# Performance work log

Measured on AMD Instinct MI355X. Metric: run time of the kernel, lower is better.

The kernel has to match this reference:

```python
import jax, jax.numpy as jnp
import numpy as np

B, S, D_MODEL, H = 2, 2048, 768, 12
HD = D_MODEL // H  # head_dim = 64
EPS = 1e-5


def setup_inputs() -> dict:
    key = jax.random.key(0)
    ks = jax.random.split(key, 5)
    sc = 0.02
    return {
        "x": jax.random.normal(ks[0], (B, S, D_MODEL), dtype=jnp.float32),
        "Wproj_w": jax.random.normal(ks[1], (7 * D_MODEL, D_MODEL), dtype=jnp.float32) * sc,
        "Wproj_b": jax.random.normal(ks[2], (7 * D_MODEL,), dtype=jnp.float32) * sc,
        "gn_w": jnp.ones((D_MODEL,), dtype=jnp.float32),
        "gn_b": jnp.zeros((D_MODEL,), dtype=jnp.float32),
        "out_w": jax.random.normal(ks[3], (D_MODEL, D_MODEL), dtype=jnp.float32) * sc,
        "out_b": jax.random.normal(ks[4], (D_MODEL,), dtype=jnp.float32) * sc,
    }


def _time_swiglu(qkv):
    # qkv: [B, S, 7, H, D]
    q1, k1, q2, k2, q3, k3, v = [qkv[:, :, i] for i in range(7)]
    a1 = jnp.einsum('bthd,bshd->bhts', q1, k1)  # [B,H,S,S], raw scores, no softmax
    a2 = jnp.einsum('bthd,bshd->bhts', q2, k2)
    a3 = jnp.einsum('bthd,bshd->bhts', q3, k3)
    t1 = jax.nn.silu(jnp.einsum('bhts,bshd->bthd', a1, v))
    t2 = jnp.einsum('bhts,bshd->bthd', a2, v)
    return jnp.einsum('bhts,bshd->bthd', a3, t1 * t2)  # [B,S,H,D]


def _group_norm(ctx, gn_w, gn_b):
    # ctx: [B, S, D_MODEL]; torch applies GroupNorm(H, D_MODEL) over (B, C=D_MODEL, L=S)
    g = ctx.reshape(B, S, H, HD)
    mean = jnp.mean(g, axis=(1, 3), keepdims=True)          # per (batch, group) over (S, HD)
    var = jnp.var(g, axis=(1, 3), keepdims=True)
    g = (g - mean) * jax.lax.rsqrt(var + EPS)
    g = g.reshape(B, S, D_MODEL)
    return g * gn_w + gn_b


def reference(x, Wproj_w, Wproj_b, gn_w, gn_b, out_w, out_b):
    qkv = x @ Wproj_w.T + Wproj_b                  # [B,S,7*D_MODEL]
    qkv = qkv.reshape(B, S, 7, H, HD)
    ctx = _time_swiglu(qkv).reshape(B, S, D_MODEL)  # [B,S,D_MODEL]
    ctx = _group_norm(ctx, gn_w, gn_b)
    return ctx @ out_w.T + out_b
```

## Files before the change

### kernel.cpp

```cpp
#include <hip/hip_runtime.h>
#include <hip/hip_bf16.h>
#include <stdint.h>

typedef short short8 __attribute__((ext_vector_type(8)));
typedef float f32x4 __attribute__((ext_vector_type(4)));
typedef unsigned short u16x4 __attribute__((ext_vector_type(4)));

#define MFMA16 __builtin_amdgcn_mfma_f32_16x16x32_bf16

typedef unsigned int __attribute__((address_space(1))) as1_u32;
typedef unsigned int __attribute__((address_space(3))) as3_u32;
#define GLOAD16(gsrc, ldst) \
  __builtin_amdgcn_global_load_lds((const as1_u32*)(gsrc), (as3_u32*)(ldst), 16, 0, 0)

__device__ __forceinline__ unsigned short f2bf(float f) {
  __hip_bfloat16 h = __float2bfloat16(f);
  return *(unsigned short*)&h;
}

__global__ __launch_bounds__(256) void cvt_bf16_4(const float* __restrict__ in,
                                                  unsigned short* __restrict__ out,
                                                  int n) {
  int i = (blockIdx.x * 256 + threadIdx.x) * 4;
  if (i >= n) return;
  f32x4 v = *(const f32x4*)(in + i);
  u16x4 o;
  o.x = f2bf(v.x); o.y = f2bf(v.y); o.z = f2bf(v.z); o.w = f2bf(v.w);
  *(u16x4*)(out + i) = o;
}

__global__ __launch_bounds__(256) void transp64(const unsigned short* __restrict__ src,
                                                int stride, int off,
                                                unsigned short* __restrict__ dst) {
  __shared__ __align__(16) unsigned short t[64 * 64];
  const int tid = threadIdx.x;
  const int tt = blockIdx.x, bh = blockIdx.y;
  const int b = bh / 12, h = bh % 12;
  const unsigned short* sbase = src + (size_t)(b * 2048 + tt * 64) * stride + h * 64 + off;
  for (int it = 0; it < 2; ++it) {
    int slot = it * 256 + tid, s = slot >> 3, j = slot & 7;
    short8 v = *(const short8*)(sbase + (size_t)s * stride + j * 8);
    int phys = (s + 8 * j) & 63;
    for (int e = 0; e < 8; ++e)
      t[(j * 8 + e) * 64 + phys] = ((unsigned short*)&v)[e];
  }
  __syncthreads();
  unsigned short* dbase = dst + (size_t)bh * 64 * 2048 + tt * 64;
  for (int it = 0; it < 2; ++it) {
    int slot = it * 256 + tid, d = slot >> 3, c = slot & 7;
    int pc = (c + (d >> 3)) & 7;
    short8 v = *(const short8*)(t + d * 64 + pc * 8);
    *(short8*)(dbase + (size_t)d * 2048 + c * 8) = v;
  }
}

template <bool OUT_BF16>
__global__ __launch_bounds__(256) void gemm_nt(const unsigned short* __restrict__ A,
                                               const unsigned short* __restrict__ Bm,
                                               const float* __restrict__ bias,
                                               void* __restrict__ Cout,
                                               int M, int N, int K) {
  __shared__ __align__(16) char smem[32768];
  char* As = smem;
  char* Bs = smem + 16384;
  const int tid = threadIdx.x;
  const int w = tid >> 6, l = tid & 63;
  const int wm = w >> 1, wn = w & 1;
  const int Row0 = blockIdx.y * 128, Col0 = blockIdx.x * 128;

  f32x4 z; z.x = 0.f; z.y = 0.f; z.z = 0.f; z.w = 0.f;
  f32x4 acc[4][4];
  for (int m = 0; m < 4; ++m)
    for (int n = 0; n < 4; ++n) acc[m][n] = z;

  for (int k0 = 0; k0 < K; k0 += 64) {
    for (int it = 0; it < 4; ++it) {
      int slot = it * 256 + tid;
      int row = slot >> 3, j = slot & 7;
      int gc = j ^ (row & 7);
      GLOAD16(A + (size_t)(Row0 + row) * K + k0 + gc * 8, As + slot * 16);
      GLOAD16(Bm + (size_t)(Col0 + row) * K + k0 + gc * 8, Bs + slot * 16);
    }
    __syncthreads();
    for (int kc = 0; kc < 2; ++kc) {
      int c = (l >> 4) + 4 * kc;
      short8 af[4], bf[4];
      for (int m = 0; m < 4; ++m) {
        int t = wm * 64 + m * 16 + (l & 15);
        af[m] = *(const short8*)(As + t * 128 + ((c ^ (t & 7)) * 16));
      }
      for (int n = 0; n < 4; ++n) {
        int t = wn * 64 + n * 16 + (l & 15);
        bf[n] = *(const short8*)(Bs + t * 128 + ((c ^ (t & 7)) * 16));
      }
      for (int m = 0; m < 4; ++m)
        for (int n = 0; n < 4; ++n)
          acc[m][n] = MFMA16(af[m], bf[n], acc[m][n], 0, 0, 0);
    }
    __syncthreads();
  }
  for (int n = 0; n < 4; ++n) {
    int col = Col0 + wn * 64 + n * 16 + (l & 15);
    float bv = bias[col];
    for (int m = 0; m < 4; ++m) {
      int rbase = Row0 + wm * 64 + m * 16 + (l >> 4) * 4;
      for (int r = 0; r < 4; ++r) {
        float v = acc[m][n][r] + bv;
        size_t idx = (size_t)(rbase + r) * N + col;
        if (OUT_BF16) ((unsigned short*)Cout)[idx] = f2bf(v);
        else          ((float*)Cout)[idx] = v;
      }
    }
  }
}

__global__ __launch_bounds__(256) void pass1(const unsigned short* __restrict__ qkv,
                                             const unsigned short* __restrict__ vt,
                                             unsigned short* __restrict__ u) {
  __shared__ __align__(16) char smem[40960];
  char* K1s = smem;
  char* K2s = smem + 8192;
  char* Vts = smem + 16384;
  char* A1s = smem + 24576;
  char* A2s = smem + 32768;
  const int tid = threadIdx.x, w = tid >> 6, l = tid & 63;
  const int tt = blockIdx.x;
  const int bh = blockIdx.y;
  const int b = bh / 12, h = bh % 12;

  const int tg = tt * 64 + w * 16 + (l & 15);
  const size_t qbase = (size_t)(b * 2048 + tg) * 5376 + h * 64;
  short8 q1f[2], q2f[2];
  for (int kc = 0; kc < 2; ++kc) {
    int d = kc * 32 + (l >> 4) * 8;
    q1f[kc] = *(const short8*)(qkv + qbase + 0 * 768 + d);
    q2f[kc] = *(const short8*)(qkv + qbase + 2 * 768 + d);
  }

  f32x4 z; z.x = 0.f; z.y = 0.f; z.z = 0.f; z.w = 0.f;
  f32x4 t1a[4], t2a[4];
  for (int n = 0; n < 4; ++n) { t1a[n] = z; t2a[n] = z; }

  for (int s0 = 0; s0 < 2048; s0 += 64) {
    for (int it = 0; it < 2; ++it) {
      int slot = it * 256 + tid;
      int row = slot >> 3, j = slot & 7;
      int gc = j ^ (row & 7);
      const unsigned short* k1src = qkv + (size_t)(b * 2048 + s0 + row) * 5376 + h * 64 + 768 + gc * 8;
      GLOAD16(k1src, K1s + slot * 16);
      GLOAD16(k1src + 2 * 768, K2s + slot * 16);
      GLOAD16(vt + (size_t)(bh * 64 + row) * 2048 + s0 + gc * 8, Vts + slot * 16);
    }
    __syncthreads();

    f32x4 a1[4], a2[4];
    for (int n = 0; n < 4; ++n) { a1[n] = z; a2[n] = z; }
    for (int kc = 0; kc < 2; ++kc) {
      int c = (l >> 4) + 4 * kc;
      for (int n = 0; n < 4; ++n) {
        int srw = n * 16 + (l & 15);
        short8 k1f = *(const short8*)(K1s + srw * 128 + ((c ^ (srw & 7)) * 16));
        short8 k2f = *(const short8*)(K2s + srw * 128 + ((c ^ (srw & 7)) * 16));
        a1[n] = MFMA16(q1f[kc], k1f, a1[n], 0, 0, 0);
        a2[n] = MFMA16(q2f[kc], k2f, a2[n], 0, 0, 0);
      }
    }

    char* myA1 = A1s + w * 2048;
    char* myA2 = A2s + w * 2048;
    for (int n = 0; n < 4; ++n)
      for (int r = 0; r < 4; ++r) {
        int trow = (l >> 4) * 4 + r;
        int scol = n * 16 + (l & 15);
        int byte = trow * 128 + (((scol >> 3) ^ (trow & 7)) * 16) + (scol & 7) * 2;
        *(unsigned short*)(myA1 + byte) = f2bf(a1[n][r]);
        *(unsigned short*)(myA2 + byte) = f2bf(a2[n][r]);
      }
    __syncthreads();

    for (int kc = 0; kc < 2; ++kc) {
      int trow = l & 15;
      int c = (l >> 4) + 4 * kc;
      short8 p1 = *(const short8*)(myA1 + trow * 128 + ((c ^ (trow & 7)) * 16));
      short8 p2 = *(const short8*)(myA2 + trow * 128 + ((c ^ (trow & 7)) * 16));
      for (int n = 0; n < 4; ++n) {
        int drow = n * 16 + (l & 15);
        short8 vf = *(const short8*)(Vts + drow * 128 + ((c ^ (drow & 7)) * 16));
        t1a[n] = MFMA16(p1, vf, t1a[n], 0, 0, 0);
        t2a[n] = MFMA16(p2, vf, t2a[n], 0, 0, 0);
      }
    }
    __syncthreads();
  }

  for (int n = 0; n < 4; ++n)
    for (int r = 0; r < 4; ++r) {
      int t = tt * 64 + w * 16 + (l >> 4) * 4 + r;
      int d = n * 16 + (l & 15);
      float x1 = t1a[n][r], x2 = t2a[n][r];
      float uu = (x1 / (1.f + expf(-x1))) * x2;
      u[(size_t)(b * 2048 + t) * 768 + h * 64 + d] = f2bf(uu);
    }
}

__global__ __launch_bounds__(256) void pass2(const unsigned short* __restrict__ qkv,
                                             const unsigned short* __restrict__ ut,
                                             float* __restrict__ ctx,
                                             float* __restrict__ partials) {
  __shared__ __align__(16) char smem[24576];
  char* K3s = smem;
  char* Uts = smem + 8192;
  char* A3s = smem + 16384;
  const int tid = threadIdx.x, w = tid >> 6, l = tid & 63;
  const int tt = blockIdx.x;
  const int bh = blockIdx.y;
  const int b = bh / 12, h = bh % 12;

  const int tg = tt * 64 + w * 16 + (l & 15);
  const size_t qbase = (size_t)(b * 2048 + tg) * 5376 + h * 64;
  short8 q3f[2];
  for (int kc = 0; kc < 2; ++kc)
    q3f[kc] = *(const short8*)(qkv + qbase + 4 * 768 + kc * 32 + (l >> 4) * 8);

  f32x4 z; z.x = 0.f; z.y = 0.f; z.z = 0.f; z.w = 0.f;
  f32x4 ca[4];
  for (int n = 0; n < 4; ++n) ca[n] = z;

  for (int s0 = 0; s0 < 2048; s0 += 64) {
    for (int it = 0; it < 2; ++it) {
      int slot = it * 256 + tid;
      int row = slot >> 3, j = slot & 7;
      int gc = j ^ (row & 7);
      GLOAD16(qkv + (size_t)(b * 2048 + s0 + row) * 5376 + h * 64 + 5 * 768 + gc * 8,
              K3s + slot * 16);
      GLOAD16(ut + (size_t)(bh * 64 + row) * 2048 + s0 + gc * 8, Uts + slot * 16);
    }
    __syncthreads();

    f32x4 a3[4];
    for (int n = 0; n < 4; ++n) a3[n] = z;
    for (int kc = 0; kc < 2; ++kc) {
      int c = (l >> 4) + 4 * kc;
      for (int n = 0; n < 4; ++n) {
        int srw = n * 16 + (l & 15);
        short8 kf = *(const short8*)(K3s + srw * 128 + ((c ^ (srw & 7)) * 16));
        a3[n] = MFMA16(q3f[kc], kf, a3[n], 0, 0, 0);
      }
    }
    char* myA = A3s + w * 2048;
    for (int n = 0; n < 4; ++n)
      for (int r = 0; r < 4; ++r) {
        int trow = (l >> 4) * 4 + r;
        int scol = n * 16 + (l & 15);
        int byte = trow * 128 + (((scol >> 3) ^ (trow & 7)) * 16) + (scol & 7) * 2;
        *(unsigned short*)(myA + byte) = f2bf(a3[n][r]);
      }
    __syncthreads();

    for (int kc = 0; kc < 2; ++kc) {
      int trow = l & 15;
      int c = (l >> 4) + 4 * kc;
      short8 p3 = *(const short8*)(myA + trow * 128 + ((c ^ (trow & 7)) * 16));
      for (int n = 0; n < 4; ++n) {
        int drow = n * 16 + (l & 15);
        short8 uf = *(const short8*)(Uts + drow * 128 + ((c ^ (drow & 7)) * 16));
        ca[n] = MFMA16(p3, uf, ca[n], 0, 0, 0);
      }
    }
    __syncthreads();
  }

  float psum = 0.f, psum2 = 0.f;
  for (int n = 0; n < 4; ++n)
    for (int r = 0; r < 4; ++r) {
      int t = tt * 64 + w * 16 + (l >> 4) * 4 + r;
      int d = n * 16 + (l & 15);
      float v = ca[n][r];
      ctx[(size_t)(b * 2048 + t) * 768 + h * 64 + d] = v;
      psum += v; psum2 += v * v;
    }

  float* red = (float*)smem;
  red[tid] = psum; red[256 + tid] = psum2;
  __syncthreads();
  for (int st = 128; st > 0; st >>= 1) {
    if (tid < st) {
      red[tid] += red[tid + st];
      red[256 + tid] += red[256 + tid + st];
    }
    __syncthreads();
  }
  if (tid == 0) {
    partials[(bh * 32 + tt) * 2] = red[0];
    partials[(bh * 32 + tt) * 2 + 1] = red[256];
  }
}

__global__ __launch_bounds__(64) void gn_finalize(const float* __restrict__ partials,
                                                  float* __restrict__ stats) {
  const int g = blockIdx.x;
  const int l = threadIdx.x;
  double s = 0.0, s2 = 0.0;
  if (l < 32) {
    s = (double)partials[(g * 32 + l) * 2];
    s2 = (double)partials[(g * 32 + l) * 2 + 1];
  }
  for (int off = 32; off > 0; off >>= 1) {
    s += __shfl_down(s, off, 64);
    s2 += __shfl_down(s2, off, 64);
  }
  if (l == 0) {
    const double N = 2048.0 * 64.0;
    double mean = s / N;
    double var = s2 / N - mean * mean;
    stats[g * 2] = (float)mean;
    stats[g * 2 + 1] = (float)(1.0 / sqrt(var + 1e-5));
  }
}

__global__ __launch_bounds__(256) void gn_apply(const float* __restrict__ ctx,
                                                const float* __restrict__ stats,
                                                const float* __restrict__ gw,
                                                const float* __restrict__ gb,
                                                unsigned short* __restrict__ outc) {
  int i = blockIdx.x * 256 + threadIdx.x;
  if (i >= 4096 * 768) return;
  int c = i % 768;
  int b = i / (2048 * 768);
  int g = b * 12 + (c >> 6);
  float v = (ctx[i] - stats[2 * g]) * stats[2 * g + 1];
  outc[i] = f2bf(v * gw[c] + gb[c]);
}

extern "C" void kernel_launch(void* const* d_in, const int* in_sizes, int n_in,
                              void* d_out, int out_size, void* d_ws, size_t ws_size,
                              hipStream_t stream) {
  const float* x   = (const float*)d_in[0];
  const float* Wpw = (const float*)d_in[1];
  const float* Wpb = (const float*)d_in[2];
  const float* gnw = (const float*)d_in[3];
  const float* gnb = (const float*)d_in[4];
  const float* ow  = (const float*)d_in[5];
  const float* ob  = (const float*)d_in[6];
  float* out = (float*)d_out;

  char* ws = (char*)d_ws;
  size_t off = 0;
  auto carve = [&](size_t bytes) {
    char* p = ws + off;
    off = (off + bytes + 255) & ~(size_t)255;
    return p;
  };
  unsigned short* xb   = (unsigned short*)carve((size_t)4096 * 768 * 2);
  unsigned short* wb   = (unsigned short*)carve((size_t)5376 * 768 * 2);
  unsigned short* owb  = (unsigned short*)carve((size_t)768 * 768 * 2);
  unsigned short* qkvb = (unsigned short*)carve((size_t)4096 * 5376 * 2);
  unsigned short* ub   = (unsigned short*)carve((size_t)4096 * 768 * 2);
  unsigned short* vtb  = (unsigned short*)carve((size_t)24 * 64 * 2048 * 2);
  unsigned short* utb  = (unsigned short*)carve((size_t)24 * 64 * 2048 * 2);
  float* ctx           = (float*)carve((size_t)4096 * 768 * 4);
  float* partials      = (float*)carve(24 * 32 * 2 * 4);
  float* stats         = (float*)carve(48 * 4);

  cvt_bf16_4<<<3072, 256, 0, stream>>>(x, xb, 4096 * 768);
  cvt_bf16_4<<<4032, 256, 0, stream>>>(Wpw, wb, 5376 * 768);
  cvt_bf16_4<<<576, 256, 0, stream>>>(ow, owb, 768 * 768);

  gemm_nt<true><<<dim3(42, 32), 256, 0, stream>>>(xb, wb, Wpb, qkvb, 4096, 5376, 768);
  transp64<<<dim3(32, 24), 256, 0, stream>>>(qkvb, 5376, 6 * 768, vtb);
  pass1<<<dim3(32, 24), 256, 0, stream>>>(qkvb, vtb, ub);
  transp64<<<dim3(32, 24), 256, 0, stream>>>(ub, 768, 0, utb);
  pass2<<<dim3(32, 24), 256, 0, stream>>>(qkvb, utb, ctx, partials);
  gn_finalize<<<24, 64, 0, stream>>>(partials, stats);
  gn_apply<<<12288, 256, 0, stream>>>(ctx, stats, gnw, gnb, xb);
  gemm_nt<false><<<dim3(6, 32), 256, 0, stream>>>(xb, owb, ob, out, 4096, 768, 768);
}
```

Measured before the change: 238.1 us.

## Switch attention passes to 32x32 MFMA with 128-row query tiles per block

Both attention passes move from 16x16x32 to 32x32x16 bf16 MFMA. Each wave now owns 32 query rows, so a block covers 128 rows and the grid halves from 32 to 16 tiles per head. Each staged K/V/U tile is therefore reused across twice as many queries, and global traffic per output is lower. The score tile is computed transposed (K as the A operand) so it can be written to LDS as packed 64-bit stores. The mid-loop block barrier is replaced by a per-wave lgkmcnt wait, since each wave only reads its own score region. The trade-off is fewer blocks (384), more LDS per block and more accumulator registers, which may reduce occupancy.

```diff
diff --git a/kernel.cpp b/kernel.cpp
--- a/kernel.cpp
+++ b/kernel.cpp
@@ -4,9 +4,11 @@
 
 typedef short short8 __attribute__((ext_vector_type(8)));
 typedef float f32x4 __attribute__((ext_vector_type(4)));
+typedef float f32x16 __attribute__((ext_vector_type(16)));
 typedef unsigned short u16x4 __attribute__((ext_vector_type(4)));
 
 #define MFMA16 __builtin_amdgcn_mfma_f32_16x16x32_bf16
+#define MFMA32 __builtin_amdgcn_mfma_f32_32x32x16_bf16
 
 typedef unsigned int __attribute__((address_space(1))) as1_u32;
 typedef unsigned int __attribute__((address_space(3))) as3_u32;
@@ -16,6 +18,9 @@
 __device__ __forceinline__ unsigned short f2bf(float f) {
   __hip_bfloat16 h = __float2bfloat16(f);
   return *(unsigned short*)&h;
+}
+__device__ __forceinline__ unsigned pk2(float lo, float hi) {
+  return ((unsigned)f2bf(hi) << 16) | (unsigned)f2bf(lo);
 }
 
 __global__ __launch_bounds__(256) void cvt_bf16_4(const float* __restrict__ in,
@@ -117,87 +122,103 @@
 __global__ __launch_bounds__(256) void pass1(const unsigned short* __restrict__ qkv,
                                              const unsigned short* __restrict__ vt,
                                              unsigned short* __restrict__ u) {
-  __shared__ __align__(16) char smem[40960];
+  __shared__ __align__(16) char smem[57344];
   char* K1s = smem;
   char* K2s = smem + 8192;
   char* Vts = smem + 16384;
   char* A1s = smem + 24576;
-  char* A2s = smem + 32768;
+  char* A2s = smem + 40960;
   const int tid = threadIdx.x, w = tid >> 6, l = tid & 63;
-  const int tt = blockIdx.x;
-  const int bh = blockIdx.y;
+  const int g5 = l >> 5, l31 = l & 31;
+  const int tt = blockIdx.x, bh = blockIdx.y;
   const int b = bh / 12, h = bh % 12;
 
-  const int tg = tt * 64 + w * 16 + (l & 15);
-  const size_t qbase = (size_t)(b * 2048 + tg) * 5376 + h * 64;
-  short8 q1f[2], q2f[2];
-  for (int kc = 0; kc < 2; ++kc) {
-    int d = kc * 32 + (l >> 4) * 8;
-    q1f[kc] = *(const short8*)(qkv + qbase + 0 * 768 + d);
-    q2f[kc] = *(const short8*)(qkv + qbase + 2 * 768 + d);
-  }
-
-  f32x4 z; z.x = 0.f; z.y = 0.f; z.z = 0.f; z.w = 0.f;
-  f32x4 t1a[4], t2a[4];
-  for (int n = 0; n < 4; ++n) { t1a[n] = z; t2a[n] = z; }
+  const int tg = tt * 128 + w * 32 + l31;
+  const unsigned short* qrow = qkv + (size_t)(b * 2048 + tg) * 5376 + h * 64;
+  short8 q1f[4], q2f[4];
+#pragma unroll
+  for (int kc = 0; kc < 4; ++kc) {
+    int d = kc * 16 + g5 * 8;
+    q1f[kc] = *(const short8*)(qrow + 0 * 768 + d);
+    q2f[kc] = *(const short8*)(qrow + 2 * 768 + d);
+  }
+
+  f32x16 z16;
+#pragma unroll
+  for (int i = 0; i < 16; ++i) z16[i] = 0.f;
+  f32x16 t1a[2], t2a[2];
+  t1a[0] = z16; t1a[1] = z16; t2a[0] = z16; t2a[1] = z16;
+
+  char* myA1 = A1s + w * 4096;
+  char* myA2 = A2s + w * 4096;
 
   for (int s0 = 0; s0 < 2048; s0 += 64) {
+#pragma unroll
     for (int it = 0; it < 2; ++it) {
       int slot = it * 256 + tid;
       int row = slot >> 3, j = slot & 7;
       int gc = j ^ (row & 7);
-      const unsigned short* k1src = qkv + (size_t)(b * 2048 + s0 + row) * 5376 + h * 64 + 768 + gc * 8;
-      GLOAD16(k1src, K1s + slot * 16);
-      GLOAD16(k1src + 2 * 768, K2s + slot * 16);
+      const unsigned short* ksrc =
+          qkv + (size_t)(b * 2048 + s0 + row) * 5376 + h * 64 + 768 + gc * 8;
+      GLOAD16(ksrc, K1s + slot * 16);
+      GLOAD16(ksrc + 2 * 768, K2s + slot * 16);
       GLOAD16(vt + (size_t)(bh * 64 + row) * 2048 + s0 + gc * 8, Vts + slot * 16);
     }
     __syncthreads();
 
-    f32x4 a1[4], a2[4];
-    for (int n = 0; n < 4; ++n) { a1[n] = z; a2[n] = z; }
-    for (int kc = 0; kc < 2; ++kc) {
-      int c = (l >> 4) + 4 * kc;
-      for (int n = 0; n < 4; ++n) {
-        int srw = n * 16 + (l & 15);
-        short8 k1f = *(const short8*)(K1s + srw * 128 + ((c ^ (srw & 7)) * 16));
-        short8 k2f = *(const short8*)(K2s + srw * 128 + ((c ^ (srw & 7)) * 16));
-        a1[n] = MFMA16(q1f[kc], k1f, a1[n], 0, 0, 0);
-        a2[n] = MFMA16(q2f[kc], k2f, a2[n], 0, 0, 0);
-      }
-    }
-
-    char* myA1 = A1s + w * 2048;
-    char* myA2 = A2s + w * 2048;
-    for (int n = 0; n < 4; ++n)
-      for (int r = 0; r < 4; ++r) {
-        int trow = (l >> 4) * 4 + r;
-        int scol = n * 16 + (l & 15);
-        int byte = trow * 128 + (((scol >> 3) ^ (trow & 7)) * 16) + (scol & 7) * 2;
-        *(unsigned short*)(myA1 + byte) = f2bf(a1[n][r]);
-        *(unsigned short*)(myA2 + byte) = f2bf(a2[n][r]);
-      }
-    __syncthreads();
-
-    for (int kc = 0; kc < 2; ++kc) {
-      int trow = l & 15;
-      int c = (l >> 4) + 4 * kc;
-      short8 p1 = *(const short8*)(myA1 + trow * 128 + ((c ^ (trow & 7)) * 16));
-      short8 p2 = *(const short8*)(myA2 + trow * 128 + ((c ^ (trow & 7)) * 16));
-      for (int n = 0; n < 4; ++n) {
-        int drow = n * 16 + (l & 15);
-        short8 vf = *(const short8*)(Vts + drow * 128 + ((c ^ (drow & 7)) * 16));
-        t1a[n] = MFMA16(p1, vf, t1a[n], 0, 0, 0);
-        t2a[n] = MFMA16(p2, vf, t2a[n], 0, 0, 0);
-      }
-    }
-    __syncthreads();
-  }
-
-  for (int n = 0; n < 4; ++n)
-    for (int r = 0; r < 4; ++r) {
-      int t = tt * 64 + w * 16 + (l >> 4) * 4 + r;
-      int d = n * 16 + (l & 15);
-      float x1 = t1a[n][r], x2 = t2a[n][r];
+    f32x16 a1t[2], a2t[2];
+    a1t[0] = z16; a1t[1] = z16; a2t[0] = z16; a2t[1] = z16;
+#pragma unroll
+    for (int kc = 0; kc < 4; ++kc) {
+#pragma unroll
+      for (int n = 0; n < 2; ++n) {
+        int srow = n * 32 + l31;
+        int off = srow * 128 + (((kc * 2 + g5) ^ (srow & 7)) * 16);
+        a1t[n] = MFMA32(*(const short8*)(K1s + off), q1f[kc], a1t[n], 0, 0, 0);
+        a2t[n] = MFMA32(*(const short8*)(K2s + off), q2f[kc], a2t[n], 0, 0, 0);
+      }
+    }
+
+#pragma unroll
+    for (int n = 0; n < 2; ++n)
+#pragma unroll
+      for (int rq = 0; rq < 4; ++rq) {
+        int sbase = n * 32 + rq * 8 + g5 * 4;
+        int byte = l31 * 128 + (((sbase >> 3) ^ (l31 & 7)) * 16) + (sbase & 7) * 2;
+        uint2 w1, w2;
+        w1.x = pk2(a1t[n][rq * 4], a1t[n][rq * 4 + 1]);
+        w1.y = pk2(a1t[n][rq * 4 + 2], a1t[n][rq * 4 + 3]);
+        w2.x = pk2(a2t[n][rq * 4], a2t[n][rq * 4 + 1]);
+        w2.y = pk2(a2t[n][rq * 4 + 2], a2t[n][rq * 4 + 3]);
+        *(uint2*)(myA1 + byte) = w1;
+        *(uint2*)(myA2 + byte) = w2;
+      }
+    asm volatile("s_waitcnt lgkmcnt(0)" ::: "memory");
+
+#pragma unroll
+    for (int kc2 = 0; kc2 < 4; ++kc2) {
+      int chunk = kc2 * 2 + g5;
+      int aoff = l31 * 128 + ((chunk ^ (l31 & 7)) * 16);
+      short8 pa1 = *(const short8*)(myA1 + aoff);
+      short8 pa2 = *(const short8*)(myA2 + aoff);
+#pragma unroll
+      for (int dn = 0; dn < 2; ++dn) {
+        int drow = dn * 32 + l31;
+        short8 vf = *(const short8*)(Vts + drow * 128 + ((chunk ^ (drow & 7)) * 16));
+        t1a[dn] = MFMA32(pa1, vf, t1a[dn], 0, 0, 0);
+        t2a[dn] = MFMA32(pa2, vf, t2a[dn], 0, 0, 0);
+      }
+    }
+    __syncthreads();
+  }
+
+#pragma unroll
+  for (int dn = 0; dn < 2; ++dn)
+#pragma unroll
+    for (int r = 0; r < 16; ++r) {
+      int t = tt * 128 + w * 32 + (r & 3) + 8 * (r >> 2) + 4 * g5;
+      int d = dn * 32 + l31;
+      float x1 = t1a[dn][r], x2 = t2a[dn][r];
       float uu = (x1 / (1.f + expf(-x1))) * x2;
       u[(size_t)(b * 2048 + t) * 768 + h * 64 + d] = f2bf(uu);
     }
@@ -207,26 +228,31 @@
                                              const unsigned short* __restrict__ ut,
                                              float* __restrict__ ctx,
                                              float* __restrict__ partials) {
-  __shared__ __align__(16) char smem[24576];
+  __shared__ __align__(16) char smem[32768];
   char* K3s = smem;
   char* Uts = smem + 8192;
   char* A3s = smem + 16384;
   const int tid = threadIdx.x, w = tid >> 6, l = tid & 63;
-  const int tt = blockIdx.x;
-  const int bh = blockIdx.y;
+  const int g5 = l >> 5, l31 = l & 31;
+  const int tt = blockIdx.x, bh = blockIdx.y;
   const int b = bh / 12, h = bh % 12;
 
-  const int tg = tt * 64 + w * 16 + (l & 15);
-  const size_t qbase = (size_t)(b * 2048 + tg) * 5376 + h * 64;
-  short8 q3f[2];
-  for (int kc = 0; kc < 2; ++kc)
-    q3f[kc] = *(const short8*)(qkv + qbase + 4 * 768 + kc * 32 + (l >> 4) * 8);
-
-  f32x4 z; z.x = 0.f; z.y = 0.f; z.z = 0.f; z.w = 0.f;
-  f32x4 ca[4];
-  for (int n = 0; n < 4; ++n) ca[n] = z;
+  const int tg = tt * 128 + w * 32 + l31;
+  const unsigned short* qrow = qkv + (size_t)(b * 2048 + tg) * 5376 + h * 64;
+  short8 q3f[4];
+#pragma unroll
+  for (int kc = 0; kc < 4; ++kc)
+    q3f[kc] = *(const short8*)(qrow + 4 * 768 + kc * 16 + g5 * 8);
+
+  f32x16 z16;
+#pragma unroll
+  for (int i = 0; i < 16; ++i) z16[i] = 0.f;
+  f32x16 ca[2];
+  ca[0] = z16; ca[1] = z16;
+  char* myA = A3s + w * 4096;
 
   for (int s0 = 0; s0 < 2048; s0 += 64) {
+#pragma unroll
     for (int it = 0; it < 2; ++it) {
       int slot = it * 256 + tid;
       int row = slot >> 3, j = slot & 7;
@@ -237,45 +263,52 @@
     }
     __syncthreads();
 
-    f32x4 a3[4];
-    for (int n = 0; n < 4; ++n) a3[n] = z;
-    for (int kc = 0; kc < 2; ++kc) {
-      int c = (l >> 4) + 4 * kc;
-      for (int n = 0; n < 4; ++n) {
-        int srw = n * 16 + (l & 15);
-        short8 kf = *(const short8*)(K3s + srw * 128 + ((c ^ (srw & 7)) * 16));
-        a3[n] = MFMA16(q3f[kc], kf, a3[n], 0, 0, 0);
-      }
-    }
-    char* myA = A3s + w * 2048;
-    for (int n = 0; n < 4; ++n)
-      for (int r = 0; r < 4; ++r) {
-        int trow = (l >> 4) * 4 + r;
-        int scol = n * 16 + (l & 15);
-        int byte = trow * 128 + (((scol >> 3) ^ (trow & 7)) * 16) + (scol & 7) * 2;
-        *(unsigned short*)(myA + byte) = f2bf(a3[n][r]);
-      }
-    __syncthreads();
-
-    for (int kc = 0; kc < 2; ++kc) {
-      int trow = l & 15;
-      int c = (l >> 4) + 4 * kc;
-      short8 p3 = *(const short8*)(myA + trow * 128 + ((c ^ (trow & 7)) * 16));
-      for (int n = 0; n < 4; ++n) {
-        int drow = n * 16 + (l & 15);
-        short8 uf = *(const short8*)(Uts + drow * 128 + ((c ^ (drow & 7)) * 16));
-        ca[n] = MFMA16(p3, uf, ca[n], 0, 0, 0);
+    f32x16 a3t[2];
+    a3t[0] = z16; a3t[1] = z16;
+#pragma unroll
+    for (int kc = 0; kc < 4; ++kc) {
+#pragma unroll
+      for (int n = 0; n < 2; ++n) {
+        int srow = n * 32 + l31;
+        int off = srow * 128 + (((kc * 2 + g5) ^ (srow & 7)) * 16);
+        a3t[n] = MFMA32(*(const short8*)(K3s + off), q3f[kc], a3t[n], 0, 0, 0);
+      }
+    }
+#pragma unroll
+    for (int n = 0; n < 2; ++n)
+#pragma unroll
+      for (int rq = 0; rq < 4; ++rq) {
+        int sbase = n * 32 + rq * 8 + g5 * 4;
+        int byte = l31 * 128 + (((sbase >> 3) ^ (l31 & 7)) * 16) + (sbase & 7) * 2;
+        uint2 w1;
+        w1.x = pk2(a3t[n][rq * 4], a3t[n][rq * 4 + 1]);
+        w1.y = pk2(a3t[n][rq * 4 + 2], a3t[n][rq * 4 + 3]);
+        *(uint2*)(myA + byte) = w1;
+      }
+    asm volatile("s_waitcnt lgkmcnt(0)" ::: "memory");
+
+#pragma unroll
+    for (int kc2 = 0; kc2 < 4; ++kc2) {
+      int chunk = kc2 * 2 + g5;
+      short8 pa = *(const short8*)(myA + l31 * 128 + ((chunk ^ (l31 & 7)) * 16));
+#pragma unroll
+      for (int dn = 0; dn < 2; ++dn) {
+        int drow = dn * 32 + l31;
+        short8 uf = *(const short8*)(Uts + drow * 128 + ((chunk ^ (drow & 7)) * 16));
+        ca[dn] = MFMA32(pa, uf, ca[dn], 0, 0, 0);
       }
     }
     __syncthreads();
   }
 
   float psum = 0.f, psum2 = 0.f;
-  for (int n = 0; n < 4; ++n)
-    for (int r = 0; r < 4; ++r) {
-      int t = tt * 64 + w * 16 + (l >> 4) * 4 + r;
-      int d = n * 16 + (l & 15);
-      float v = ca[n][r];
+#pragma unroll
+  for (int dn = 0; dn < 2; ++dn)
+#pragma unroll
+    for (int r = 0; r < 16; ++r) {
+      int t = tt * 128 + w * 32 + (r & 3) + 8 * (r >> 2) + 4 * g5;
+      int d = dn * 32 + l31;
+      float v = ca[dn][r];
       ctx[(size_t)(b * 2048 + t) * 768 + h * 64 + d] = v;
       psum += v; psum2 += v * v;
     }
@@ -291,8 +324,8 @@
     __syncthreads();
   }
   if (tid == 0) {
-    partials[(bh * 32 + tt) * 2] = red[0];
-    partials[(bh * 32 + tt) * 2 + 1] = red[256];
+    partials[(bh * 16 + tt) * 2] = red[0];
+    partials[(bh * 16 + tt) * 2 + 1] = red[256];
   }
 }
 
@@ -301,9 +334,9 @@
   const int g = blockIdx.x;
   const int l = threadIdx.x;
   double s = 0.0, s2 = 0.0;
-  if (l < 32) {
-    s = (double)partials[(g * 32 + l) * 2];
-    s2 = (double)partials[(g * 32 + l) * 2 + 1];
+  if (l < 16) {
+    s = (double)partials[(g * 16 + l) * 2];
+    s2 = (double)partials[(g * 16 + l) * 2 + 1];
   }
   for (int off = 32; off > 0; off >>= 1) {
     s += __shfl_down(s, off, 64);
@@ -359,7 +392,7 @@
   unsigned short* vtb  = (unsigned short*)carve((size_t)24 * 64 * 2048 * 2);
   unsigned short* utb  = (unsigned short*)carve((size_t)24 * 64 * 2048 * 2);
   float* ctx           = (float*)carve((size_t)4096 * 768 * 4);
-  float* partials      = (float*)carve(24 * 32 * 2 * 4);
+  float* partials      = (float*)carve(24 * 16 * 2 * 4);
   float* stats         = (float*)carve(48 * 4);
 
   cvt_bf16_4<<<3072, 256, 0, stream>>>(x, xb, 4096 * 768);
@@ -368,9 +401,9 @@
 
   gemm_nt<true><<<dim3(42, 32), 256, 0, stream>>>(xb, wb, Wpb, qkvb, 4096, 5376, 768);
   transp64<<<dim3(32, 24), 256, 0, stream>>>(qkvb, 5376, 6 * 768, vtb);
-  pass1<<<dim3(32, 24), 256, 0, stream>>>(qkvb, vtb, ub);
+  pass1<<<dim3(16, 24), 256, 0, stream>>>(qkvb, vtb, ub);
   transp64<<<dim3(32, 24), 256, 0, stream>>>(ub, 768, 0, utb);
-  pass2<<<dim3(32, 24), 256, 0, stream>>>(qkvb, utb, ctx, partials);
+  pass2<<<dim3(16, 24), 256, 0, stream>>>(qkvb, utb, ctx, partials);
   gn_finalize<<<24, 64, 0, stream>>>(partials, stats);
   gn_apply<<<12288, 256, 0, stream>>>(ctx, stats, gnw, gnb, xb);
   gemm_nt<false><<<dim3(6, 32), 256, 0, stream>>>(xb, owb, ob, out, 4096, 768, 768);
```

Result: slower. 267.5 us (+12.4%).
